# Performance work log

Measured on AMD Instinct MI355X. Metric: run time of the kernel, lower is better.

The kernel has to match this reference:

```python
import jax, jax.numpy as jnp
import numpy as np
from jax import lax

LATENT_DIM = 512
UNITS = LATENT_DIM // 2  # per-direction LSTM units (Keras LSTM(latent_dim//2))
FEAT = 512


def _lstm_scan(x, W, U, b):
    """Keras-style LSTM over x: [B, T, F]. Gate order i, f, g(candidate), o.
    Returns (hs [B,T,u], h_last [B,u], c_last [B,u])."""
    B = x.shape[0]
    u = U.shape[0]
    # Precompute input projections for all timesteps (one big GEMM).
    xz = jnp.einsum('btf,fg->btg', x, W) + b  # [B, T, 4u]

    def step(carry, zt):
        h, c = carry
        z = zt + h @ U  # [B, 4u]
        i = jax.nn.sigmoid(z[:, :u])
        f = jax.nn.sigmoid(z[:, u:2 * u])
        g = jnp.tanh(z[:, 2 * u:3 * u])
        o = jax.nn.sigmoid(z[:, 3 * u:])
        c_new = f * c + i * g
        h_new = o * jnp.tanh(c_new)
        return (h_new, c_new), h_new

    init = (jnp.zeros((B, u), x.dtype), jnp.zeros((B, u), x.dtype))
    (h_last, c_last), hs = lax.scan(step, init, jnp.swapaxes(xz, 0, 1))
    return jnp.swapaxes(hs, 0, 1), h_last, c_last


def setup_inputs() -> dict:
    key = jax.random.key(0)
    ks = jax.random.split(key, 7)
    B, T, F, u = 64, 1024, FEAT, UNITS
    s_in = 1.0 / np.sqrt(F)
    s_rec = 1.0 / np.sqrt(u)
    return {
        'x': jax.random.normal(ks[0], (B, T, F), jnp.float32),
        'W_fwd': jax.random.normal(ks[1], (F, 4 * u), jnp.float32) * s_in,
        'U_fwd': jax.random.normal(ks[2], (u, 4 * u), jnp.float32) * s_rec,
        'b_fwd': jnp.zeros((4 * u,), jnp.float32),
        'W_bwd': jax.random.normal(ks[3], (F, 4 * u), jnp.float32) * s_in,
        'U_bwd': jax.random.normal(ks[4], (u, 4 * u), jnp.float32) * s_rec,
        'b_bwd': jnp.zeros((4 * u,), jnp.float32),
    }


def reference(x, W_fwd, U_fwd, b_fwd, W_bwd, U_bwd, b_bwd):
    # Forward direction
    hs_f, h_f, c_f = _lstm_scan(x, W_fwd, U_fwd, b_fwd)
    # Backward direction: process reversed sequence, re-reverse outputs (Keras Bidirectional)
    hs_b, h_b, c_b = _lstm_scan(x[:, ::-1, :], W_bwd, U_bwd, b_bwd)
    hs_b = hs_b[:, ::-1, :]
    enc_out = jnp.concatenate([hs_f, hs_b], axis=-1)  # [B, T, latent]
    h = jnp.concatenate([h_f, h_b], axis=-1)          # [B, latent]
    c = jnp.concatenate([c_f, c_b], axis=-1)          # [B, latent]
    return enc_out, h, c
```

## Files before the change

kernel.cpp:

```cpp
#include <hip/hip_runtime.h>
#include <cstdint>
#include <cstddef>

typedef _Float16 f16x2 __attribute__((ext_vector_type(2)));
typedef _Float16 half4 __attribute__((ext_vector_type(4)));
typedef _Float16 half8 __attribute__((ext_vector_type(8)));
typedef float f32x4 __attribute__((ext_vector_type(4)));

static constexpr int BB = 64;
static constexpr int TT = 1024;
static constexpr int FF = 512;
static constexpr int UU = 256;
static constexpr int NZ = 1024;

static constexpr size_t LSTM_SHBYTES = 90112;

__device__ __forceinline__ f16x2 bc16(unsigned int v) { return __builtin_bit_cast(f16x2, v); }

__device__ __forceinline__ void st_u32_rlx(unsigned int* p, unsigned int v)
{
    __hip_atomic_store(p, v, __ATOMIC_RELAXED, __HIP_MEMORY_SCOPE_AGENT);
}
__device__ __forceinline__ unsigned int ld_u32_rlx(const unsigned int* p)
{
    return __hip_atomic_load(p, __ATOMIC_RELAXED, __HIP_MEMORY_SCOPE_AGENT);
}

__device__ __forceinline__ void bar_lgkm()
{
    asm volatile("s_waitcnt lgkmcnt(0)\n\ts_barrier" ::: "memory");
}

__global__ __launch_bounds__(256) void enc_cast_x(
    const float* __restrict__ x, _Float16* __restrict__ x16, int n4)
{
    int stride = gridDim.x * 256;
    for (int i = blockIdx.x * 256 + threadIdx.x; i < n4; i += stride) {
        float4 v = ((const float4*)x)[i];
        half4 o;
        o.x = (_Float16)v.x; o.y = (_Float16)v.y;
        o.z = (_Float16)v.z; o.w = (_Float16)v.w;
        ((half4*)x16)[i] = o;
    }
}

__global__ __launch_bounds__(256) void enc_cast_wt(
    const float* __restrict__ Wf, const float* __restrict__ Wb,
    _Float16* __restrict__ WT)
{
    __shared__ float tile[64][65];
    const int t = threadIdx.x;
    const int k0 = blockIdx.x * 64;
    const int n0 = blockIdx.y * 64;
    const int d = blockIdx.z;
    const float* W = d ? Wb : Wf;
    _Float16* WTd = WT + (size_t)d * NZ * FF;
#pragma unroll
    for (int p = 0; p < 16; ++p) {
        int idx = p * 256 + t;
        int r = idx >> 6, c = idx & 63;
        tile[r][c] = W[(size_t)(k0 + r) * NZ + n0 + c];
    }
    __syncthreads();
#pragma unroll
    for (int p = 0; p < 16; ++p) {
        int idx = p * 256 + t;
        int r = idx >> 6, c = idx & 63;
        WTd[(size_t)(n0 + r) * FF + k0 + c] = (_Float16)tile[c][r];
    }
}

__global__ __launch_bounds__(256) void enc_pack_u16v2(
    const float* __restrict__ Uf, const float* __restrict__ Ub,
    uint4* __restrict__ Upkr2)
{
    int idx = blockIdx.x * 256 + threadIdx.x;
    if (idx >= 2 * 128 * 256) return;
    int d  = idx >> 15;
    int k2 = (idx >> 8) & 127;
    int j  = idx & 255;
    int k = 2 * k2;
    const float* Ud = d ? Ub : Uf;
    unsigned int w[4];
#pragma unroll
    for (int g = 0; g < 4; ++g) {
        f16x2 h;
        h.x = (_Float16)Ud[(size_t)k * NZ + g * 256 + j];
        h.y = (_Float16)Ud[(size_t)(k + 1) * NZ + g * 256 + j];
        w[g] = __builtin_bit_cast(unsigned int, h);
    }
    Upkr2[idx] = make_uint4(w[0], w[1], w[2], w[3]);
}

__global__ __launch_bounds__(256) void enc_zero(float* __restrict__ p, int n)
{
    int i = blockIdx.x * 256 + threadIdx.x;
    if (i < n) p[i] = 0.f;
}

__global__ __launch_bounds__(256) void enc_gemm16(
    const _Float16* __restrict__ x16, const _Float16* __restrict__ WT,
    const float* __restrict__ bf, const float* __restrict__ bb,
    _Float16* __restrict__ xz16, int c0, int CT)
{
    __shared__ __align__(16) _Float16 Ash[128][40];
    __shared__ __align__(16) _Float16 Bsh[128][40];

    const int t = threadIdx.x;
    const int r0 = blockIdx.x * 128;
    const int n0 = blockIdx.y * 128;
    const int MperD = BB * CT;
    const int d = r0 / MperD;

    const int srow = t >> 2;
    const int koff = (t & 3) * 8;

    auto xrowptr = [&](int r) -> const _Float16* {
        int rd = r - d * MperD;
        int b = rd / CT;
        int tl = rd - b * CT;
        int tsrc = d ? (TT - 1 - (c0 + tl)) : (c0 + tl);
        return x16 + ((size_t)b * TT + tsrc) * FF;
    };
    const _Float16* ap0 = xrowptr(r0 + srow);
    const _Float16* ap1 = xrowptr(r0 + 64 + srow);
    const _Float16* wp0 = WT + (size_t)(d * NZ + n0 + srow) * FF;
    const _Float16* wp1 = wp0 + (size_t)64 * FF;

    const int lane = t & 63;
    const int w = t >> 6;
    const int wm = w >> 1, wn = w & 1;
    const int l15 = lane & 15;
    const int kq = (lane >> 4) * 8;

    f32x4 acc[4][4];
#pragma unroll
    for (int i = 0; i < 4; ++i)
#pragma unroll
        for (int j = 0; j < 4; ++j) acc[i][j] = (f32x4)0.f;

    for (int ks = 0; ks < FF / 32; ++ks) {
        const int k0 = ks * 32;
        uint4 av0 = *(const uint4*)(ap0 + k0 + koff);
        uint4 av1 = *(const uint4*)(ap1 + k0 + koff);
        uint4 bv0 = *(const uint4*)(wp0 + k0 + koff);
        uint4 bv1 = *(const uint4*)(wp1 + k0 + koff);
        __syncthreads();
        *(uint4*)&Ash[srow][koff]      = av0;
        *(uint4*)&Ash[64 + srow][koff] = av1;
        *(uint4*)&Bsh[srow][koff]      = bv0;
        *(uint4*)&Bsh[64 + srow][koff] = bv1;
        __syncthreads();

        half8 af[4], bfr[4];
#pragma unroll
        for (int mf = 0; mf < 4; ++mf)
            af[mf] = *(const half8*)&Ash[wm * 64 + mf * 16 + l15][kq];
#pragma unroll
        for (int nf = 0; nf < 4; ++nf)
            bfr[nf] = *(const half8*)&Bsh[wn * 64 + nf * 16 + l15][kq];
#pragma unroll
        for (int mf = 0; mf < 4; ++mf)
#pragma unroll
            for (int nf = 0; nf < 4; ++nf)
                acc[mf][nf] = __builtin_amdgcn_mfma_f32_16x16x32_f16(
                    af[mf], bfr[nf], acc[mf][nf], 0, 0, 0);
    }

    const float* bd = d ? bb : bf;
    const int rbase = r0 + wm * 64;
    const int cbase = n0 + wn * 64;
#pragma unroll
    for (int nf = 0; nf < 4; ++nf) {
        const int cc = cbase + nf * 16 + l15;
        const float bia = bd[cc];
#pragma unroll
        for (int mf = 0; mf < 4; ++mf) {
#pragma unroll
            for (int rg = 0; rg < 4; ++rg) {
                int rr = rbase + mf * 16 + (lane >> 4) * 4 + rg;
                xz16[(size_t)rr * NZ + cc] = (_Float16)(acc[mf][nf][rg] + bia);
            }
        }
    }
}

__device__ __forceinline__ float sigm_f(float xv)
{
    return 1.0f / (1.0f + __expf(-xv));
}
__device__ __forceinline__ float tanh_f(float xv)
{
    return 2.0f / (1.0f + __expf(-2.0f * xv)) - 1.0f;
}

__global__ __launch_bounds__(512, 2) void enc_lstm_split(
    const _Float16* __restrict__ xz16, const uint4* __restrict__ Upkr2,
    float* __restrict__ hstate, float* __restrict__ cstate,
    unsigned int* __restrict__ hbuf,
    float* __restrict__ out, int c0, int CT)
{
    extern __shared__ char smem2[];
    float4*    parts = (float4*)smem2;
    _Float16*  hsh   = (_Float16*)(smem2 + 8192);
    uint4*     hshq  = (uint4*)hsh;

    const int t  = threadIdx.x;
    const int s  = t >> 7;
    const int jl = t & 127;
    const int beta = blockIdx.x;
    const int jh = beta >> 7;
    const int c  = beta & 127;
    const int d  = c >> 6;
    const int b  = c & 63;
    const int j  = jh * 128 + jl;
    const int partner = beta ^ 128;
    const bool own = ((s >> 1) == jh);
    const bool isx = (s == (jh ? 1 : 2));

    const uint4* Uq = Upkr2 + ((size_t)d * 128 + s * 32) * 256 + j;
    f16x2 ureg[32][4];
#pragma unroll
    for (int m = 0; m < 32; ++m) {
        uint4 qv = Uq[(size_t)m * 256];
        ureg[m][0] = bc16(qv.x);
        ureg[m][1] = bc16(qv.y);
        ureg[m][2] = bc16(qv.z);
        ureg[m][3] = bc16(qv.w);
    }

    float cr = 0.f, hn = 0.f;
    if (s == 0) cr = cstate[(size_t)c * UU + j];
    if (t < 256) hsh[t] = (_Float16)hstate[(size_t)c * UU + t];
    __syncthreads();

    const _Float16* xzrow = xz16 + (size_t)c * CT * NZ;
    float* outb = out + (size_t)b * TT * (2 * UU) + d * UU;

    unsigned short xp0 = 0, xp1 = 0, xp2 = 0, xp3 = 0;
    if (s == 0) {
        const unsigned short* p = (const unsigned short*)xzrow + j;
        xp0 = p[0]; xp1 = p[256]; xp2 = p[512]; xp3 = p[768];
    }
    unsigned int pref = 0;

    auto dot4 = [&](float& a0, float& a1, float& a2, float& a3) {
#pragma unroll
        for (int r = 0; r < 8; ++r) {
            uint4 hq = hshq[s * 8 + r];
            f16x2 hw[4] = {bc16(hq.x), bc16(hq.y), bc16(hq.z), bc16(hq.w)};
#pragma unroll
            for (int q = 0; q < 4; ++q) {
                const int m = r * 4 + q;
                a0 = __builtin_amdgcn_fdot2(hw[q], ureg[m][0], a0, false);
                a1 = __builtin_amdgcn_fdot2(hw[q], ureg[m][1], a1, false);
                a2 = __builtin_amdgcn_fdot2(hw[q], ureg[m][2], a2, false);
                a3 = __builtin_amdgcn_fdot2(hw[q], ureg[m][3], a3, false);
            }
        }
    };

    for (int tl = 0; tl < CT; ++tl) {
        const int step = c0 + tl + 1;
        const int htag = c0 + tl;

        if (own) {
            float a0 = 0.f, a1 = 0.f, a2 = 0.f, a3 = 0.f;
            dot4(a0, a1, a2, a3);
            parts[s * 128 + jl] = make_float4(a0, a1, a2, a3);
        }
        if (isx && tl > 0) {
            const unsigned int* pp =
                &hbuf[((size_t)(htag & 1) * 256 + partner) * 128 + jl];
            unsigned int v = pref;
            while ((v >> 16) != (unsigned int)htag)
                v = ld_u32_rlx(pp);
            hsh[(1 - jh) * 128 + jl] =
                __builtin_bit_cast(_Float16, (unsigned short)(v & 0xffffu));
        }
        bar_lgkm();

        if (!own) {
            float a0 = 0.f, a1 = 0.f, a2 = 0.f, a3 = 0.f;
            dot4(a0, a1, a2, a3);
            parts[s * 128 + jl] = make_float4(a0, a1, a2, a3);
        }
        bar_lgkm();

        if (s == 0) {
            float4 p0 = parts[jl], p1 = parts[128 + jl];
            float4 p2 = parts[256 + jl], p3 = parts[384 + jl];
            float zi = p0.x + p1.x + p2.x + p3.x
                     + (float)__builtin_bit_cast(_Float16, xp0);
            float zf = p0.y + p1.y + p2.y + p3.y
                     + (float)__builtin_bit_cast(_Float16, xp1);
            float zg = p0.z + p1.z + p2.z + p3.z
                     + (float)__builtin_bit_cast(_Float16, xp2);
            float zo = p0.w + p1.w + p2.w + p3.w
                     + (float)__builtin_bit_cast(_Float16, xp3);
            float ig = sigm_f(zi), fg = sigm_f(zf), gg = tanh_f(zg), og = sigm_f(zo);
            cr = fg * cr + ig * gg;
            hn = og * tanh_f(cr);
            _Float16 h16 = (_Float16)hn;
            st_u32_rlx(&hbuf[((size_t)(step & 1) * 256 + beta) * 128 + jl],
                       ((unsigned int)step << 16)
                       | (unsigned int)__builtin_bit_cast(unsigned short, h16));
            hsh[j] = h16;
            int tsrc = d ? (TT - 1 - (c0 + tl)) : (c0 + tl);
            outb[(size_t)tsrc * (2 * UU) + j] = hn;
            int tn = (tl + 1 < CT) ? tl + 1 : tl;
            const unsigned short* pn =
                (const unsigned short*)(xzrow + (size_t)tn * NZ) + j;
            xp0 = pn[0]; xp1 = pn[256]; xp2 = pn[512]; xp3 = pn[768];
        }
        if (isx) {
            pref = ld_u32_rlx(&hbuf[((size_t)(step & 1) * 256 + partner) * 128 + jl]);
        }
        bar_lgkm();
    }

    if (s == 0) {
        hstate[(size_t)c * UU + j] = hn;
        cstate[(size_t)c * UU + j] = cr;
    }
}

__global__ __launch_bounds__(256) void enc_final(
    const float* __restrict__ hstate, const float* __restrict__ cstate,
    float* __restrict__ out)
{
    int idx = blockIdx.x * 256 + threadIdx.x;
    if (idx >= 2 * BB * UU) return;
    int d = idx / (BB * UU);
    int rem = idx - d * (BB * UU);
    int b = rem / UU;
    int j = rem - b * UU;
    size_t OUT_H = (size_t)BB * TT * (2 * UU);
    size_t HSZ = (size_t)BB * (2 * UU);
    out[OUT_H + (size_t)b * (2 * UU) + d * UU + j] = hstate[idx];
    out[OUT_H + HSZ + (size_t)b * (2 * UU) + d * UU + j] = cstate[idx];
}

extern "C" void kernel_launch(void* const* d_in, const int* in_sizes, int n_in,
                              void* d_out, int out_size, void* d_ws, size_t ws_size,
                              hipStream_t stream)
{
    const float* x  = (const float*)d_in[0];
    const float* Wf = (const float*)d_in[1];
    const float* Uf = (const float*)d_in[2];
    const float* bf = (const float*)d_in[3];
    const float* Wb = (const float*)d_in[4];
    const float* Ub = (const float*)d_in[5];
    const float* bb = (const float*)d_in[6];
    float* out = (float*)d_out;

    const size_t x16_bytes   = (size_t)BB * TT * FF * 2;
    const size_t wt_bytes    = (size_t)2 * NZ * FF * 2;
    const size_t upk_bytes   = (size_t)2 * 128 * 256 * sizeof(uint4);
    const size_t state_bytes = (size_t)2 * BB * UU * sizeof(float);
    const size_t hbuf_bytes  = (size_t)2 * 256 * 128 * 4;
    const size_t fixed = x16_bytes + wt_bytes + upk_bytes + 2 * state_bytes
                       + hbuf_bytes;

    int CT = TT;
    while (CT > 8) {
        size_t need = fixed + (size_t)2 * BB * CT * NZ * 2;
        if (need <= ws_size) break;
        CT >>= 1;
    }

    char* wsb = (char*)d_ws;
    _Float16* x16 = (_Float16*)wsb;
    _Float16* WT  = (_Float16*)(wsb + x16_bytes);
    uint4* Upkr2  = (uint4*)(wsb + x16_bytes + wt_bytes);
    float* hstate = (float*)(wsb + x16_bytes + wt_bytes + upk_bytes);
    float* cstate = hstate + 2 * BB * UU;
    unsigned int* hbuf = (unsigned int*)(wsb + x16_bytes + wt_bytes + upk_bytes
                                         + 2 * state_bytes);
    _Float16* xz16 = (_Float16*)(wsb + fixed);

    (void)hipFuncSetAttribute(reinterpret_cast<const void*>(enc_lstm_split),
                              hipFuncAttributeMaxDynamicSharedMemorySize,
                              (int)LSTM_SHBYTES);

    enc_cast_x<<<4096, 256, 0, stream>>>(x, x16, BB * TT * FF / 4);
    enc_cast_wt<<<dim3(8, 16, 2), 256, 0, stream>>>(Wf, Wb, WT);
    enc_pack_u16v2<<<(2 * 128 * 256 + 255) / 256, 256, 0, stream>>>(Uf, Ub, Upkr2);
    enc_zero<<<(2 * 2 * BB * UU + 255) / 256, 256, 0, stream>>>(hstate, 2 * 2 * BB * UU);

    for (int c0 = 0; c0 < TT; c0 += CT) {
        dim3 ggrid((2 * BB * CT) / 128, NZ / 128);
        enc_gemm16<<<ggrid, 256, 0, stream>>>(x16, WT, bf, bb, xz16, c0, CT);
        enc_lstm_split<<<256, 512, LSTM_SHBYTES, stream>>>(
            xz16, Upkr2, hstate, cstate, hbuf, out, c0, CT);
    }
    enc_final<<<(2 * BB * UU + 255) / 256, 256, 0, stream>>>(hstate, cstate, out);
}
```

Baseline: 1.692 ms.

## Split recurrent dot across quad lanes with DPP reduction, drop a barrier

Restructures the LSTM recurrence so each group of 4 adjacent lanes splits the k-dimension for one hidden unit and reduces the partial sums with DPP cross-lane moves instead of through shared memory. This removes the partial-sum LDS round trip and one of the two block barriers per timestep, and every thread now computes gates redundantly. The h vector is replicated into four padded LDS copies so the quads read without bank conflicts. The x-projection load moves into the loop as a per-step load.

Result: slower. 1.751 ms (+3.5%).

```diff
diff --git a/kernel.cpp b/kernel.cpp
--- a/kernel.cpp
+++ b/kernel.cpp
@@ -14,6 +14,7 @@
 static constexpr int NZ = 1024;
 
 static constexpr size_t LSTM_SHBYTES = 90112;
+static constexpr int HREP_STRIDE = 608;
 
 __device__ __forceinline__ f16x2 bc16(unsigned int v) { return __builtin_bit_cast(f16x2, v); }
 
@@ -29,6 +30,15 @@
 __device__ __forceinline__ void bar_lgkm()
 {
     asm volatile("s_waitcnt lgkmcnt(0)\n\ts_barrier" ::: "memory");
+}
+
+__device__ __forceinline__ float qsum(float v)
+{
+    int b1 = __builtin_amdgcn_mov_dpp(__builtin_bit_cast(int, v), 0xB1, 0xf, 0xf, true);
+    v += __builtin_bit_cast(float, b1);
+    int b2 = __builtin_amdgcn_mov_dpp(__builtin_bit_cast(int, v), 0x4E, 0xf, 0xf, true);
+    v += __builtin_bit_cast(float, b2);
+    return v;
 }
 
 __global__ __launch_bounds__(256) void enc_cast_x(
@@ -185,6 +195,25 @@
     }
 }
 
+template <int MBASE>
+__device__ __forceinline__ void dot16(const uint4 (&ureg)[32], const char* hptr,
+                                      float& a0, float& a1, float& a2, float& a3)
+{
+#pragma unroll
+    for (int r = 0; r < 4; ++r) {
+        uint4 hq = *(const uint4*)(hptr + r * 16);
+#pragma unroll
+        for (int e = 0; e < 4; ++e) {
+            f16x2 hw = bc16((&hq.x)[e]);
+            const uint4 uv = ureg[MBASE + r * 4 + e];
+            a0 = __builtin_amdgcn_fdot2(hw, bc16(uv.x), a0, false);
+            a1 = __builtin_amdgcn_fdot2(hw, bc16(uv.y), a1, false);
+            a2 = __builtin_amdgcn_fdot2(hw, bc16(uv.z), a2, false);
+            a3 = __builtin_amdgcn_fdot2(hw, bc16(uv.w), a3, false);
+        }
+    }
+}
+
 __device__ __forceinline__ float sigm_f(float xv)
 {
     return 1.0f / (1.0f + __expf(-xv));
@@ -194,20 +223,18 @@
     return 2.0f / (1.0f + __expf(-2.0f * xv)) - 1.0f;
 }
 
-__global__ __launch_bounds__(512, 2) void enc_lstm_split(
+__global__ __launch_bounds__(512, 2) void enc_lstm_quad(
     const _Float16* __restrict__ xz16, const uint4* __restrict__ Upkr2,
     float* __restrict__ hstate, float* __restrict__ cstate,
     unsigned int* __restrict__ hbuf,
     float* __restrict__ out, int c0, int CT)
 {
     extern __shared__ char smem2[];
-    float4*    parts = (float4*)smem2;
-    _Float16*  hsh   = (_Float16*)(smem2 + 8192);
-    uint4*     hshq  = (uint4*)hsh;
 
     const int t  = threadIdx.x;
-    const int s  = t >> 7;
-    const int jl = t & 127;
+    const int q  = t & 3;
+    const int jl = t >> 2;
+    const int w  = t >> 6;
     const int beta = blockIdx.x;
     const int jh = beta >> 7;
     const int c  = beta & 127;
@@ -215,111 +242,90 @@
     const int b  = c & 63;
     const int j  = jh * 128 + jl;
     const int partner = beta ^ 128;
-    const bool own = ((s >> 1) == jh);
-    const bool isx = (s == (jh ? 1 : 2));
-
-    const uint4* Uq = Upkr2 + ((size_t)d * 128 + s * 32) * 256 + j;
-    f16x2 ureg[32][4];
-#pragma unroll
-    for (int m = 0; m < 32; ++m) {
-        uint4 qv = Uq[(size_t)m * 256];
-        ureg[m][0] = bc16(qv.x);
-        ureg[m][1] = bc16(qv.y);
-        ureg[m][2] = bc16(qv.z);
-        ureg[m][3] = bc16(qv.w);
-    }
-
-    float cr = 0.f, hn = 0.f;
-    if (s == 0) cr = cstate[(size_t)c * UU + j];
-    if (t < 256) hsh[t] = (_Float16)hstate[(size_t)c * UU + t];
+
+    const uint4* Uq = Upkr2 + (size_t)d * 128 * 256 + j;
+    uint4 ureg[32];
+#pragma unroll
+    for (int m = 0; m < 16; ++m)
+        ureg[m] = Uq[(size_t)(q * 16 + m) * 256];
+#pragma unroll
+    for (int m = 0; m < 16; ++m)
+        ureg[16 + m] = Uq[(size_t)(64 + q * 16 + m) * 256];
+
+    float cr = cstate[(size_t)c * UU + j];
+    float hn = 0.f;
+    if (t < 256) {
+        _Float16 hv = (_Float16)hstate[(size_t)c * UU + t];
+        *(unsigned short*)(smem2 + ((t & 127) >> 5) * HREP_STRIDE + t * 2) =
+            __builtin_bit_cast(unsigned short, hv);
+    }
     __syncthreads();
 
     const _Float16* xzrow = xz16 + (size_t)c * CT * NZ;
     float* outb = out + (size_t)b * TT * (2 * UU) + d * UU;
 
-    unsigned short xp0 = 0, xp1 = 0, xp2 = 0, xp3 = 0;
-    if (s == 0) {
-        const unsigned short* p = (const unsigned short*)xzrow + j;
-        xp0 = p[0]; xp1 = p[256]; xp2 = p[512]; xp3 = p[768];
-    }
+    const char* hp0 = smem2 + q * HREP_STRIDE + (0 * 16 + q * 4) * 16;
+    const char* hp1 = smem2 + q * HREP_STRIDE + (1 * 16 + q * 4) * 16;
+
+    const int al = t - 384;
+    const int pj = (1 - jh) * 128 + (al & 127);
     unsigned int pref = 0;
-
-    auto dot4 = [&](float& a0, float& a1, float& a2, float& a3) {
-#pragma unroll
-        for (int r = 0; r < 8; ++r) {
-            uint4 hq = hshq[s * 8 + r];
-            f16x2 hw[4] = {bc16(hq.x), bc16(hq.y), bc16(hq.z), bc16(hq.w)};
-#pragma unroll
-            for (int q = 0; q < 4; ++q) {
-                const int m = r * 4 + q;
-                a0 = __builtin_amdgcn_fdot2(hw[q], ureg[m][0], a0, false);
-                a1 = __builtin_amdgcn_fdot2(hw[q], ureg[m][1], a1, false);
-                a2 = __builtin_amdgcn_fdot2(hw[q], ureg[m][2], a2, false);
-                a3 = __builtin_amdgcn_fdot2(hw[q], ureg[m][3], a3, false);
-            }
-        }
-    };
 
     for (int tl = 0; tl < CT; ++tl) {
         const int step = c0 + tl + 1;
         const int htag = c0 + tl;
 
-        if (own) {
-            float a0 = 0.f, a1 = 0.f, a2 = 0.f, a3 = 0.f;
-            dot4(a0, a1, a2, a3);
-            parts[s * 128 + jl] = make_float4(a0, a1, a2, a3);
-        }
-        if (isx && tl > 0) {
+        const unsigned short xq =
+            *((const unsigned short*)(xzrow + (size_t)tl * NZ) + q * 256 + j);
+
+        if (w >= 6 && tl > 0) {
             const unsigned int* pp =
-                &hbuf[((size_t)(htag & 1) * 256 + partner) * 128 + jl];
+                &hbuf[((size_t)(htag & 1) * 256 + partner) * 128 + al];
             unsigned int v = pref;
             while ((v >> 16) != (unsigned int)htag)
                 v = ld_u32_rlx(pp);
-            hsh[(1 - jh) * 128 + jl] =
-                __builtin_bit_cast(_Float16, (unsigned short)(v & 0xffffu));
-        }
+            *(unsigned short*)(smem2 + (al >> 5) * HREP_STRIDE + pj * 2) =
+                (unsigned short)(v & 0xffffu);
+        }
+
+        float a0 = 0.f, a1 = 0.f, a2 = 0.f, a3 = 0.f;
+        if (jh == 0) dot16<0>(ureg, hp0, a0, a1, a2, a3);
+        else         dot16<16>(ureg, hp1, a0, a1, a2, a3);
         bar_lgkm();
 
-        if (!own) {
-            float a0 = 0.f, a1 = 0.f, a2 = 0.f, a3 = 0.f;
-            dot4(a0, a1, a2, a3);
-            parts[s * 128 + jl] = make_float4(a0, a1, a2, a3);
-        }
-        bar_lgkm();
-
-        if (s == 0) {
-            float4 p0 = parts[jl], p1 = parts[128 + jl];
-            float4 p2 = parts[256 + jl], p3 = parts[384 + jl];
-            float zi = p0.x + p1.x + p2.x + p3.x
-                     + (float)__builtin_bit_cast(_Float16, xp0);
-            float zf = p0.y + p1.y + p2.y + p3.y
-                     + (float)__builtin_bit_cast(_Float16, xp1);
-            float zg = p0.z + p1.z + p2.z + p3.z
-                     + (float)__builtin_bit_cast(_Float16, xp2);
-            float zo = p0.w + p1.w + p2.w + p3.w
-                     + (float)__builtin_bit_cast(_Float16, xp3);
-            float ig = sigm_f(zi), fg = sigm_f(zf), gg = tanh_f(zg), og = sigm_f(zo);
-            cr = fg * cr + ig * gg;
-            hn = og * tanh_f(cr);
-            _Float16 h16 = (_Float16)hn;
+        if (jh == 0) dot16<16>(ureg, hp1, a0, a1, a2, a3);
+        else         dot16<0>(ureg, hp0, a0, a1, a2, a3);
+
+        {
+            float xv = (float)__builtin_bit_cast(_Float16, xq);
+            a0 += (q == 0) ? xv : 0.f;
+            a1 += (q == 1) ? xv : 0.f;
+            a2 += (q == 2) ? xv : 0.f;
+            a3 += (q == 3) ? xv : 0.f;
+        }
+        float zi = qsum(a0), zf = qsum(a1), zg = qsum(a2), zo = qsum(a3);
+
+        float ig = sigm_f(zi), fg = sigm_f(zf), gg = tanh_f(zg), og = sigm_f(zo);
+        cr = fg * cr + ig * gg;
+        hn = og * tanh_f(cr);
+        _Float16 h16 = (_Float16)hn;
+        unsigned short hbits = __builtin_bit_cast(unsigned short, h16);
+
+        if (q == 0) {
             st_u32_rlx(&hbuf[((size_t)(step & 1) * 256 + beta) * 128 + jl],
-                       ((unsigned int)step << 16)
-                       | (unsigned int)__builtin_bit_cast(unsigned short, h16));
-            hsh[j] = h16;
+                       ((unsigned int)step << 16) | (unsigned int)hbits);
             int tsrc = d ? (TT - 1 - (c0 + tl)) : (c0 + tl);
             outb[(size_t)tsrc * (2 * UU) + j] = hn;
-            int tn = (tl + 1 < CT) ? tl + 1 : tl;
-            const unsigned short* pn =
-                (const unsigned short*)(xzrow + (size_t)tn * NZ) + j;
-            xp0 = pn[0]; xp1 = pn[256]; xp2 = pn[512]; xp3 = pn[768];
-        }
-        if (isx) {
-            pref = ld_u32_rlx(&hbuf[((size_t)(step & 1) * 256 + partner) * 128 + jl]);
+            *(unsigned short*)(smem2 + (jl >> 5) * HREP_STRIDE + j * 2) = hbits;
+        }
+        if (w >= 6) {
+            pref = ld_u32_rlx(
+                &hbuf[((size_t)(step & 1) * 256 + partner) * 128 + al]);
         }
         bar_lgkm();
     }
 
-    if (s == 0) {
+    if (q == 0) {
         hstate[(size_t)c * UU + j] = hn;
         cstate[(size_t)c * UU + j] = cr;
     }
@@ -379,7 +385,7 @@
                                          + 2 * state_bytes);
     _Float16* xz16 = (_Float16*)(wsb + fixed);
 
-    (void)hipFuncSetAttribute(reinterpret_cast<const void*>(enc_lstm_split),
+    (void)hipFuncSetAttribute(reinterpret_cast<const void*>(enc_lstm_quad),
                               hipFuncAttributeMaxDynamicSharedMemorySize,
                               (int)LSTM_SHBYTES);
 
@@ -391,7 +397,7 @@
     for (int c0 = 0; c0 < TT; c0 += CT) {
         dim3 ggrid((2 * BB * CT) / 128, NZ / 128);
         enc_gemm16<<<ggrid, 256, 0, stream>>>(x16, WT, bf, bb, xz16, c0, CT);
-        enc_lstm_split<<<256, 512, LSTM_SHBYTES, stream>>>(
+        enc_lstm_quad<<<256, 512, LSTM_SHBYTES, stream>>>(
             xz16, Upkr2, hstate, cstate, hbuf, out, c0, CT);
     }
     enc_final<<<(2 * BB * UU + 255) / 256, 256, 0, stream>>>(hstate, cstate, out);
```

## Split recurrent weights between registers and LDS, run one block per CU

Applied to the files above, without the earlier changes.

The recurrent U slice, previously held in 128 registers per thread, is now split: 14 dwordx4 stay in registers and 18 go into a large LDS buffer read every step. Launch bounds drop from 2 blocks to 1 per CU, which frees registers and allows the roughly 150KB of LDS. Slice 0 also keeps its own partial sum in registers instead of writing it to the parts buffer and reading it back. The aim is to relieve register pressure or spilling in the serial recurrence, at the cost of extra LDS traffic every timestep and lower occupancy.

Result: slower. 1.740 ms (+2.8%).

```diff
diff --git a/kernel.cpp b/kernel.cpp
--- a/kernel.cpp
+++ b/kernel.cpp
@@ -6,6 +6,7 @@
 typedef _Float16 half4 __attribute__((ext_vector_type(4)));
 typedef _Float16 half8 __attribute__((ext_vector_type(8)));
 typedef float f32x4 __attribute__((ext_vector_type(4)));
+typedef unsigned int u32x4 __attribute__((ext_vector_type(4)));
 
 static constexpr int BB = 64;
 static constexpr int TT = 1024;
@@ -13,7 +14,12 @@
 static constexpr int UU = 256;
 static constexpr int NZ = 1024;
 
-static constexpr size_t LSTM_SHBYTES = 90112;
+static constexpr int UREG = 14;
+static constexpr int ULDS = 18;
+static constexpr size_t ULDS_BYTES = (size_t)ULDS * 512 * 16;
+static constexpr size_t PARTS_BYTES = 3 * 128 * 16;
+static constexpr size_t HSH_BYTES = 512;
+static constexpr size_t LSTM_SHBYTES = ULDS_BYTES + PARTS_BYTES + HSH_BYTES;
 
 __device__ __forceinline__ f16x2 bc16(unsigned int v) { return __builtin_bit_cast(f16x2, v); }
 
@@ -194,16 +200,17 @@
     return 2.0f / (1.0f + __expf(-2.0f * xv)) - 1.0f;
 }
 
-__global__ __launch_bounds__(512, 2) void enc_lstm_split(
+__global__ __launch_bounds__(512, 1) void enc_lstm_split(
     const _Float16* __restrict__ xz16, const uint4* __restrict__ Upkr2,
     float* __restrict__ hstate, float* __restrict__ cstate,
     unsigned int* __restrict__ hbuf,
     float* __restrict__ out, int c0, int CT)
 {
     extern __shared__ char smem2[];
-    float4*    parts = (float4*)smem2;
-    _Float16*  hsh   = (_Float16*)(smem2 + 8192);
-    uint4*     hshq  = (uint4*)hsh;
+    u32x4*     ulds  = (u32x4*)smem2;
+    float4*    parts = (float4*)(smem2 + ULDS_BYTES);
+    _Float16*  hsh   = (_Float16*)(smem2 + ULDS_BYTES + PARTS_BYTES);
+    u32x4*     hshq  = (u32x4*)hsh;
 
     const int t  = threadIdx.x;
     const int s  = t >> 7;
@@ -218,16 +225,20 @@
     const bool own = ((s >> 1) == jh);
     const bool isx = (s == (jh ? 1 : 2));
 
-    const uint4* Uq = Upkr2 + ((size_t)d * 128 + s * 32) * 256 + j;
-    f16x2 ureg[32][4];
-#pragma unroll
-    for (int m = 0; m < 32; ++m) {
-        uint4 qv = Uq[(size_t)m * 256];
-        ureg[m][0] = bc16(qv.x);
-        ureg[m][1] = bc16(qv.y);
-        ureg[m][2] = bc16(qv.z);
-        ureg[m][3] = bc16(qv.w);
-    }
+    const u32x4* Uq = (const u32x4*)(Upkr2 + ((size_t)d * 128 + s * 32) * 256 + j);
+    u32x4 ureg[UREG];
+#pragma unroll
+    for (int m = 0; m < UREG; ++m) {
+        const u32x4* p = Uq + (size_t)m * 256;
+        asm volatile("global_load_dwordx4 %0, %1, off"
+                     : "=v"(ureg[m]) : "v"(p) : "memory");
+    }
+#pragma unroll
+    for (int m = 0; m < ULDS; ++m)
+        ulds[(size_t)m * 512 + t] = Uq[(size_t)(UREG + m) * 256];
+
+    asm volatile("s_waitcnt vmcnt(0)" ::: "memory");
+    __builtin_amdgcn_sched_barrier(0);
 
     float cr = 0.f, hn = 0.f;
     if (s == 0) cr = cstate[(size_t)c * UU + j];
@@ -244,19 +255,54 @@
     }
     unsigned int pref = 0;
 
-    auto dot4 = [&](float& a0, float& a1, float& a2, float& a3) {
-#pragma unroll
-        for (int r = 0; r < 8; ++r) {
-            uint4 hq = hshq[s * 8 + r];
-            f16x2 hw[4] = {bc16(hq.x), bc16(hq.y), bc16(hq.z), bc16(hq.w)};
-#pragma unroll
-            for (int q = 0; q < 4; ++q) {
-                const int m = r * 4 + q;
-                a0 = __builtin_amdgcn_fdot2(hw[q], ureg[m][0], a0, false);
-                a1 = __builtin_amdgcn_fdot2(hw[q], ureg[m][1], a1, false);
-                a2 = __builtin_amdgcn_fdot2(hw[q], ureg[m][2], a2, false);
-                a3 = __builtin_amdgcn_fdot2(hw[q], ureg[m][3], a3, false);
-            }
+    auto dot32 = [&](float& a0, float& a1, float& a2, float& a3) {
+        auto dotw = [&](const u32x4& uv, unsigned int hw) {
+            f16x2 h2 = bc16(hw);
+            a0 = __builtin_amdgcn_fdot2(h2, bc16(uv.x), a0, false);
+            a1 = __builtin_amdgcn_fdot2(h2, bc16(uv.y), a1, false);
+            a2 = __builtin_amdgcn_fdot2(h2, bc16(uv.z), a2, false);
+            a3 = __builtin_amdgcn_fdot2(h2, bc16(uv.w), a3, false);
+        };
+        auto L = [&](int w) -> u32x4 { return ulds[(size_t)w * 512 + t]; };
+        {
+            u32x4 hq = hshq[s * 8 + 0];
+            dotw(ureg[0], hq.x); dotw(ureg[1], hq.y);
+            dotw(ureg[2], hq.z); dotw(ureg[3], hq.w);
+        }
+        {
+            u32x4 hq = hshq[s * 8 + 1];
+            dotw(ureg[4], hq.x); dotw(ureg[5], hq.y);
+            dotw(ureg[6], hq.z); dotw(ureg[7], hq.w);
+        }
+        {
+            u32x4 hq = hshq[s * 8 + 2];
+            dotw(ureg[8], hq.x); dotw(ureg[9], hq.y);
+            dotw(ureg[10], hq.z); dotw(ureg[11], hq.w);
+        }
+        {
+            u32x4 hq = hshq[s * 8 + 3];
+            dotw(ureg[12], hq.x); dotw(ureg[13], hq.y);
+            dotw(L(0), hq.z); dotw(L(1), hq.w);
+        }
+        {
+            u32x4 hq = hshq[s * 8 + 4];
+            dotw(L(2), hq.x); dotw(L(3), hq.y);
+            dotw(L(4), hq.z); dotw(L(5), hq.w);
+        }
+        {
+            u32x4 hq = hshq[s * 8 + 5];
+            dotw(L(6), hq.x); dotw(L(7), hq.y);
+            dotw(L(8), hq.z); dotw(L(9), hq.w);
+        }
+        {
+            u32x4 hq = hshq[s * 8 + 6];
+            dotw(L(10), hq.x); dotw(L(11), hq.y);
+            dotw(L(12), hq.z); dotw(L(13), hq.w);
+        }
+        {
+            u32x4 hq = hshq[s * 8 + 7];
+            dotw(L(14), hq.x); dotw(L(15), hq.y);
+            dotw(L(16), hq.z); dotw(L(17), hq.w);
         }
     };
 
@@ -264,10 +310,10 @@
         const int step = c0 + tl + 1;
         const int htag = c0 + tl;
 
+        float a0 = 0.f, a1 = 0.f, a2 = 0.f, a3 = 0.f;
         if (own) {
-            float a0 = 0.f, a1 = 0.f, a2 = 0.f, a3 = 0.f;
-            dot4(a0, a1, a2, a3);
-            parts[s * 128 + jl] = make_float4(a0, a1, a2, a3);
+            dot32(a0, a1, a2, a3);
+            if (s) parts[(s - 1) * 128 + jl] = make_float4(a0, a1, a2, a3);
         }
         if (isx && tl > 0) {
             const unsigned int* pp =
@@ -281,22 +327,20 @@
         bar_lgkm();
 
         if (!own) {
-            float a0 = 0.f, a1 = 0.f, a2 = 0.f, a3 = 0.f;
-            dot4(a0, a1, a2, a3);
-            parts[s * 128 + jl] = make_float4(a0, a1, a2, a3);
+            dot32(a0, a1, a2, a3);
+            if (s) parts[(s - 1) * 128 + jl] = make_float4(a0, a1, a2, a3);
         }
         bar_lgkm();
 
         if (s == 0) {
-            float4 p0 = parts[jl], p1 = parts[128 + jl];
-            float4 p2 = parts[256 + jl], p3 = parts[384 + jl];
-            float zi = p0.x + p1.x + p2.x + p3.x
+            float4 p1 = parts[jl], p2 = parts[128 + jl], p3 = parts[256 + jl];
+            float zi = a0 + p1.x + p2.x + p3.x
                      + (float)__builtin_bit_cast(_Float16, xp0);
-            float zf = p0.y + p1.y + p2.y + p3.y
+            float zf = a1 + p1.y + p2.y + p3.y
                      + (float)__builtin_bit_cast(_Float16, xp1);
-            float zg = p0.z + p1.z + p2.z + p3.z
+            float zg = a2 + p1.z + p2.z + p3.z
                      + (float)__builtin_bit_cast(_Float16, xp2);
-            float zo = p0.w + p1.w + p2.w + p3.w
+            float zo = a3 + p1.w + p2.w + p3.w
                      + (float)__builtin_bit_cast(_Float16, xp3);
             float ig = sigm_f(zi), fg = sigm_f(zf), gg = tanh_f(zg), og = sigm_f(zo);
             cr = fg * cr + ig * gg;
```

## Process two sequences per LSTM block, halving grid and interleaving cross-block waits

Applied to the files above, without the earlier changes.

Each persistent LSTM block now advances two batch/direction sequences in an interleaved way, reusing the register-resident U weights for both. The grid drops from 256 to 128 blocks. The intent is that while one sequence waits on the partner block's half of h through the global hbuf handshake, the other sequence's dot products run and hide that latency. The s==0 group also keeps its own partial sum in registers instead of writing it to shared memory. The cost is twice as much serial work per block per timestep, more barriers, and fewer blocks spread across the CUs.

Measured after the change: 3.107 ms. 83.6% more time.

```diff
diff --git a/kernel.cpp b/kernel.cpp
--- a/kernel.cpp
+++ b/kernel.cpp
@@ -194,27 +194,32 @@
     return 2.0f / (1.0f + __expf(-2.0f * xv)) - 1.0f;
 }
 
-__global__ __launch_bounds__(512, 2) void enc_lstm_split(
+__global__ __launch_bounds__(512, 2) void enc_lstm_dual(
     const _Float16* __restrict__ xz16, const uint4* __restrict__ Upkr2,
     float* __restrict__ hstate, float* __restrict__ cstate,
     unsigned int* __restrict__ hbuf,
     float* __restrict__ out, int c0, int CT)
 {
     extern __shared__ char smem2[];
-    float4*    parts = (float4*)smem2;
-    _Float16*  hsh   = (_Float16*)(smem2 + 8192);
-    uint4*     hshq  = (uint4*)hsh;
+    float4*    partsA = (float4*)smem2;
+    float4*    partsB = (float4*)(smem2 + 6144);
+    _Float16*  hshA   = (_Float16*)(smem2 + 12288);
+    _Float16*  hshB   = (_Float16*)(smem2 + 12800);
+    uint4*     hshqA  = (uint4*)hshA;
+    uint4*     hshqB  = (uint4*)hshB;
 
     const int t  = threadIdx.x;
     const int s  = t >> 7;
     const int jl = t & 127;
     const int beta = blockIdx.x;
-    const int jh = beta >> 7;
-    const int c  = beta & 127;
-    const int d  = c >> 6;
-    const int b  = c & 63;
+    const int jh = beta >> 6;
+    const int p  = beta & 63;
+    const int cA = 2 * p;
+    const int cB = 2 * p + 1;
+    const int d  = cA >> 6;
+    const int bA = cA & 63;
+    const int bB = cB & 63;
     const int j  = jh * 128 + jl;
-    const int partner = beta ^ 128;
     const bool own = ((s >> 1) == jh);
     const bool isx = (s == (jh ? 1 : 2));
 
@@ -229,25 +234,36 @@
         ureg[m][3] = bc16(qv.w);
     }
 
-    float cr = 0.f, hn = 0.f;
-    if (s == 0) cr = cstate[(size_t)c * UU + j];
-    if (t < 256) hsh[t] = (_Float16)hstate[(size_t)c * UU + t];
+    float crA = 0.f, hnA = 0.f, crB = 0.f, hnB = 0.f;
+    if (s == 0) {
+        crA = cstate[(size_t)cA * UU + j];
+        crB = cstate[(size_t)cB * UU + j];
+    }
+    if (t < 256) {
+        hshA[t] = (_Float16)hstate[(size_t)cA * UU + t];
+        hshB[t] = (_Float16)hstate[(size_t)cB * UU + t];
+    }
     __syncthreads();
 
-    const _Float16* xzrow = xz16 + (size_t)c * CT * NZ;
-    float* outb = out + (size_t)b * TT * (2 * UU) + d * UU;
-
-    unsigned short xp0 = 0, xp1 = 0, xp2 = 0, xp3 = 0;
+    const _Float16* xzrowA = xz16 + (size_t)cA * CT * NZ;
+    const _Float16* xzrowB = xz16 + (size_t)cB * CT * NZ;
+    float* outbA = out + (size_t)bA * TT * (2 * UU) + d * UU;
+    float* outbB = out + (size_t)bB * TT * (2 * UU) + d * UU;
+
+    unsigned short xa0 = 0, xa1 = 0, xa2 = 0, xa3 = 0;
+    unsigned short xb0 = 0, xb1 = 0, xb2 = 0, xb3 = 0;
     if (s == 0) {
-        const unsigned short* p = (const unsigned short*)xzrow + j;
-        xp0 = p[0]; xp1 = p[256]; xp2 = p[512]; xp3 = p[768];
-    }
-    unsigned int pref = 0;
-
-    auto dot4 = [&](float& a0, float& a1, float& a2, float& a3) {
+        const unsigned short* pA = (const unsigned short*)xzrowA + j;
+        xa0 = pA[0]; xa1 = pA[256]; xa2 = pA[512]; xa3 = pA[768];
+        const unsigned short* pB = (const unsigned short*)xzrowB + j;
+        xb0 = pB[0]; xb1 = pB[256]; xb2 = pB[512]; xb3 = pB[768];
+    }
+    unsigned int prefA = 0, prefB = 0;
+
+    auto dot4 = [&](const uint4* hq_base, float& a0, float& a1, float& a2, float& a3) {
 #pragma unroll
         for (int r = 0; r < 8; ++r) {
-            uint4 hq = hshq[s * 8 + r];
+            uint4 hq = hq_base[s * 8 + r];
             f16x2 hw[4] = {bc16(hq.x), bc16(hq.y), bc16(hq.z), bc16(hq.w)};
 #pragma unroll
             for (int q = 0; q < 4; ++q) {
@@ -264,64 +280,118 @@
         const int step = c0 + tl + 1;
         const int htag = c0 + tl;
 
+        float a0 = 0.f, a1 = 0.f, a2 = 0.f, a3 = 0.f;
         if (own) {
-            float a0 = 0.f, a1 = 0.f, a2 = 0.f, a3 = 0.f;
-            dot4(a0, a1, a2, a3);
-            parts[s * 128 + jl] = make_float4(a0, a1, a2, a3);
+            dot4(hshqA, a0, a1, a2, a3);
+            if (s) partsA[(s - 1) * 128 + jl] = make_float4(a0, a1, a2, a3);
         }
         if (isx && tl > 0) {
             const unsigned int* pp =
-                &hbuf[((size_t)(htag & 1) * 256 + partner) * 128 + jl];
-            unsigned int v = pref;
+                &hbuf[((size_t)(htag & 1) * 256 + (1 - jh) * 128 + cA) * 128 + jl];
+            unsigned int v = prefA;
             while ((v >> 16) != (unsigned int)htag)
                 v = ld_u32_rlx(pp);
-            hsh[(1 - jh) * 128 + jl] =
+            hshA[(1 - jh) * 128 + jl] =
                 __builtin_bit_cast(_Float16, (unsigned short)(v & 0xffffu));
         }
         bar_lgkm();
 
         if (!own) {
-            float a0 = 0.f, a1 = 0.f, a2 = 0.f, a3 = 0.f;
-            dot4(a0, a1, a2, a3);
-            parts[s * 128 + jl] = make_float4(a0, a1, a2, a3);
+            dot4(hshqA, a0, a1, a2, a3);
+            if (s) partsA[(s - 1) * 128 + jl] = make_float4(a0, a1, a2, a3);
         }
         bar_lgkm();
 
         if (s == 0) {
-            float4 p0 = parts[jl], p1 = parts[128 + jl];
-            float4 p2 = parts[256 + jl], p3 = parts[384 + jl];
-            float zi = p0.x + p1.x + p2.x + p3.x
-                     + (float)__builtin_bit_cast(_Float16, xp0);
-            float zf = p0.y + p1.y + p2.y + p3.y
-                     + (float)__builtin_bit_cast(_Float16, xp1);
-            float zg = p0.z + p1.z + p2.z + p3.z
-                     + (float)__builtin_bit_cast(_Float16, xp2);
-            float zo = p0.w + p1.w + p2.w + p3.w
-                     + (float)__builtin_bit_cast(_Float16, xp3);
+            float4 p1 = partsA[jl], p2 = partsA[128 + jl], p3 = partsA[256 + jl];
+            float zi = a0 + p1.x + p2.x + p3.x
+                     + (float)__builtin_bit_cast(_Float16, xa0);
+            float zf = a1 + p1.y + p2.y + p3.y
+                     + (float)__builtin_bit_cast(_Float16, xa1);
+            float zg = a2 + p1.z + p2.z + p3.z
+                     + (float)__builtin_bit_cast(_Float16, xa2);
+            float zo = a3 + p1.w + p2.w + p3.w
+                     + (float)__builtin_bit_cast(_Float16, xa3);
             float ig = sigm_f(zi), fg = sigm_f(zf), gg = tanh_f(zg), og = sigm_f(zo);
-            cr = fg * cr + ig * gg;
-            hn = og * tanh_f(cr);
-            _Float16 h16 = (_Float16)hn;
-            st_u32_rlx(&hbuf[((size_t)(step & 1) * 256 + beta) * 128 + jl],
+            crA = fg * crA + ig * gg;
+            hnA = og * tanh_f(crA);
+            _Float16 h16 = (_Float16)hnA;
+            st_u32_rlx(&hbuf[((size_t)(step & 1) * 256 + jh * 128 + cA) * 128 + jl],
                        ((unsigned int)step << 16)
                        | (unsigned int)__builtin_bit_cast(unsigned short, h16));
-            hsh[j] = h16;
+            hshA[j] = h16;
             int tsrc = d ? (TT - 1 - (c0 + tl)) : (c0 + tl);
-            outb[(size_t)tsrc * (2 * UU) + j] = hn;
+            outbA[(size_t)tsrc * (2 * UU) + j] = hnA;
             int tn = (tl + 1 < CT) ? tl + 1 : tl;
             const unsigned short* pn =
-                (const unsigned short*)(xzrow + (size_t)tn * NZ) + j;
-            xp0 = pn[0]; xp1 = pn[256]; xp2 = pn[512]; xp3 = pn[768];
+                (const unsigned short*)(xzrowA + (size_t)tn * NZ) + j;
+            xa0 = pn[0]; xa1 = pn[256]; xa2 = pn[512]; xa3 = pn[768];
         }
         if (isx) {
-            pref = ld_u32_rlx(&hbuf[((size_t)(step & 1) * 256 + partner) * 128 + jl]);
+            prefB = ld_u32_rlx(
+                &hbuf[((size_t)(htag & 1) * 256 + (1 - jh) * 128 + cB) * 128 + jl]);
+        }
+        bar_lgkm();
+
+        float e0 = 0.f, e1 = 0.f, e2 = 0.f, e3 = 0.f;
+        if (own) {
+            dot4(hshqB, e0, e1, e2, e3);
+            if (s) partsB[(s - 1) * 128 + jl] = make_float4(e0, e1, e2, e3);
+        }
+        if (isx && tl > 0) {
+            const unsigned int* pp =
+                &hbuf[((size_t)(htag & 1) * 256 + (1 - jh) * 128 + cB) * 128 + jl];
+            unsigned int v = prefB;
+            while ((v >> 16) != (unsigned int)htag)
+                v = ld_u32_rlx(pp);
+            hshB[(1 - jh) * 128 + jl] =
+                __builtin_bit_cast(_Float16, (unsigned short)(v & 0xffffu));
+        }
+        bar_lgkm();
+
+        if (!own) {
+            dot4(hshqB, e0, e1, e2, e3);
+            if (s) partsB[(s - 1) * 128 + jl] = make_float4(e0, e1, e2, e3);
+        }
+        bar_lgkm();
+
+        if (s == 0) {
+            float4 p1 = partsB[jl], p2 = partsB[128 + jl], p3 = partsB[256 + jl];
+            float zi = e0 + p1.x + p2.x + p3.x
+                     + (float)__builtin_bit_cast(_Float16, xb0);
+            float zf = e1 + p1.y + p2.y + p3.y
+                     + (float)__builtin_bit_cast(_Float16, xb1);
+            float zg = e2 + p1.z + p2.z + p3.z
+                     + (float)__builtin_bit_cast(_Float16, xb2);
+            float zo = e3 + p1.w + p2.w + p3.w
+                     + (float)__builtin_bit_cast(_Float16, xb3);
+            float ig = sigm_f(zi), fg = sigm_f(zf), gg = tanh_f(zg), og = sigm_f(zo);
+            crB = fg * crB + ig * gg;
+            hnB = og * tanh_f(crB);
+            _Float16 h16 = (_Float16)hnB;
+            st_u32_rlx(&hbuf[((size_t)(step & 1) * 256 + jh * 128 + cB) * 128 + jl],
+                       ((unsigned int)step << 16)
+                       | (unsigned int)__builtin_bit_cast(unsigned short, h16));
+            hshB[j] = h16;
+            int tsrc = d ? (TT - 1 - (c0 + tl)) : (c0 + tl);
+            outbB[(size_t)tsrc * (2 * UU) + j] = hnB;
+            int tn = (tl + 1 < CT) ? tl + 1 : tl;
+            const unsigned short* pn =
+                (const unsigned short*)(xzrowB + (size_t)tn * NZ) + j;
+            xb0 = pn[0]; xb1 = pn[256]; xb2 = pn[512]; xb3 = pn[768];
+        }
+        if (isx) {
+            prefA = ld_u32_rlx(
+                &hbuf[((size_t)(step & 1) * 256 + (1 - jh) * 128 + cA) * 128 + jl]);
         }
         bar_lgkm();
     }
 
     if (s == 0) {
-        hstate[(size_t)c * UU + j] = hn;
-        cstate[(size_t)c * UU + j] = cr;
+        hstate[(size_t)cA * UU + j] = hnA;
+        cstate[(size_t)cA * UU + j] = crA;
+        hstate[(size_t)cB * UU + j] = hnB;
+        cstate[(size_t)cB * UU + j] = crB;
     }
 }
 
@@ -379,7 +449,7 @@
                                          + 2 * state_bytes);
     _Float16* xz16 = (_Float16*)(wsb + fixed);
 
-    (void)hipFuncSetAttribute(reinterpret_cast<const void*>(enc_lstm_split),
+    (void)hipFuncSetAttribute(reinterpret_cast<const void*>(enc_lstm_dual),
                               hipFuncAttributeMaxDynamicSharedMemorySize,
                               (int)LSTM_SHBYTES);
 
@@ -391,7 +461,7 @@
     for (int c0 = 0; c0 < TT; c0 += CT) {
         dim3 ggrid((2 * BB * CT) / 128, NZ / 128);
         enc_gemm16<<<ggrid, 256, 0, stream>>>(x16, WT, bf, bb, xz16, c0, CT);
-        enc_lstm_split<<<256, 512, LSTM_SHBYTES, stream>>>(
+        enc_lstm_dual<<<128, 512, LSTM_SHBYTES, stream>>>(
             xz16, Upkr2, hstate, cstate, hbuf, out, c0, CT);
     }
     enc_final<<<(2 * BB * UU + 255) / 256, 256, 0, stream>>>(hstate, cstate, out);
```
